# Optimization experiments

Hardware: AMD Instinct MI355X
Metric: run time of the kernel (lower is better)

Reference implementation:

```python
import jax, jax.numpy as jnp
import numpy as np

N = 50000
E = 800000
IN_C, HID, OUT_C = 128, 128, 40
EPS = 1e-5  # BatchNorm eps


def setup_inputs() -> dict:
    key = jax.random.key(0)
    ks = jax.random.split(key, 8)
    x = jax.random.normal(ks[0], (N, IN_C), dtype=jnp.float32)
    edge_index = jax.random.randint(ks[1], (2, E), 0, N, dtype=jnp.int64)
    s1 = 1.0 / np.sqrt(IN_C)
    s2 = 1.0 / np.sqrt(HID)
    return {
        "x": x,
        "edge_index": edge_index,
        "W1": jax.random.uniform(ks[2], (IN_C, HID), jnp.float32, -s1, s1),
        "b1": jnp.zeros((HID,), jnp.float32),
        "g1": jnp.ones((HID,), jnp.float32),
        "beta1": jnp.zeros((HID,), jnp.float32),
        "W2": jax.random.uniform(ks[3], (HID, HID), jnp.float32, -s2, s2),
        "b2": jnp.zeros((HID,), jnp.float32),
        "g2": jnp.ones((HID,), jnp.float32),
        "beta2": jnp.zeros((HID,), jnp.float32),
        "W3": jax.random.uniform(ks[4], (HID, OUT_C), jnp.float32, -s2, s2),
        "b3": jnp.zeros((OUT_C,), jnp.float32),
    }


def _gcn_norm(src, dst, num_nodes):
    # symmetric normalization D^-1/2 A D^-1/2, no self loops, unit edge weights
    deg = jax.ops.segment_sum(jnp.ones_like(dst, dtype=jnp.float32), dst,
                              num_segments=num_nodes)
    dinv = jnp.where(deg > 0, jax.lax.rsqrt(jnp.maximum(deg, 1.0)), 0.0)
    return dinv[src] * dinv[dst]  # [E]


def _conv(h, W, b, src, dst, norm, num_nodes):
    h = h @ W  # linear transform first (fewer message features)
    msg = norm[:, None] * h[src]  # [E, F] gather
    out = jax.ops.segment_sum(msg, dst, num_segments=num_nodes)  # scatter-add
    return out + b


def _bn_relu(h, g, beta):
    mu = jnp.mean(h, axis=0)
    var = jnp.mean(jnp.square(h - mu), axis=0)  # biased, as torch BN
    hn = (h - mu) * jax.lax.rsqrt(var + EPS) * g + beta
    return jax.nn.relu(hn)


def reference(x, edge_index, W1, b1, g1, beta1, W2, b2, g2, beta2, W3, b3):
    src, dst = edge_index[0], edge_index[1]
    norm = _gcn_norm(src, dst, N)  # cached=True: shared across layers
    h = _bn_relu(_conv(x, W1, b1, src, dst, norm, N), g1, beta1)
    h = _bn_relu(_conv(h, W2, b2, src, dst, norm, N), g2, beta2)
    return _conv(h, W3, b3, src, dst, norm, N)
```

## Files before the change

### kernel.cpp

```cpp
#include <hip/hip_runtime.h>
#include <hip/hip_fp16.h>

typedef _Float16 half8 __attribute__((ext_vector_type(8)));
typedef float floatx4 __attribute__((ext_vector_type(4)));


__device__ __forceinline__ void unpack8(uint4 v, float* f) {
    const __half2* hp = (const __half2*)&v;
    float2 a = __half22float2(hp[0]);
    float2 b = __half22float2(hp[1]);
    float2 c = __half22float2(hp[2]);
    float2 d = __half22float2(hp[3]);
    f[0] = a.x; f[1] = a.y; f[2] = b.x; f[3] = b.y;
    f[4] = c.x; f[5] = c.y; f[6] = d.x; f[7] = d.y;
}

__device__ __forceinline__ uint4 pack8(const float* f) {
    __half2 h0 = __floats2half2_rn(f[0], f[1]);
    __half2 h1 = __floats2half2_rn(f[2], f[3]);
    __half2 h2 = __floats2half2_rn(f[4], f[5]);
    __half2 h3 = __floats2half2_rn(f[6], f[7]);
    uint4 v;
    v.x = *(const unsigned int*)&h0;
    v.y = *(const unsigned int*)&h1;
    v.z = *(const unsigned int*)&h2;
    v.w = *(const unsigned int*)&h3;
    return v;
}

__global__ void k_zero4(float4* p, int n4) {
    int i = blockIdx.x * 256 + threadIdx.x;
    if (i < n4) p[i] = make_float4(0.f, 0.f, 0.f, 0.f);
}

__global__ void k_zeroi(int* p, int n) {
    int i = blockIdx.x * 256 + threadIdx.x;
    if (i < n) p[i] = 0;
}


__global__ void k_deg_xcd(const int* __restrict__ dst, int* __restrict__ deg,
                          int E, int rs) {
    int lo = (blockIdx.x & 7) * rs;
    int i = (blockIdx.x >> 3) * 256 + threadIdx.x;
    if (i < E) {
        int d = dst[i];
        if (d >= lo && d < lo + rs) atomicAdd(&deg[d], 1);
    }
}

__global__ void k_place_xcd(const int* __restrict__ src, const int* __restrict__ dst,
                            int* __restrict__ cursor, int* __restrict__ sidx,
                            int E, int rs) {
    int lo = (blockIdx.x & 7) * rs;
    int i = (blockIdx.x >> 3) * 256 + threadIdx.x;
    if (i < E) {
        int d = dst[i];
        if (d >= lo && d < lo + rs) {
            int pos = atomicAdd(&cursor[d], 1);
            sidx[pos] = src[i];
        }
    }
}

__global__ void k_dinv(const int* __restrict__ deg, float* __restrict__ dinv, int n) {
    int i = blockIdx.x * 256 + threadIdx.x;
    if (i < n) {
        int d = deg[i];
        dinv[i] = d > 0 ? rsqrtf((float)d) : 0.f;
    }
}

__global__ void k_blocksum(const int* __restrict__ cnt, int* __restrict__ bsum, int n) {
    __shared__ int ls[256];
    int i = blockIdx.x * 256 + threadIdx.x;
    ls[threadIdx.x] = i < n ? cnt[i] : 0;
    __syncthreads();
    for (int off = 128; off > 0; off >>= 1) {
        if (threadIdx.x < off) ls[threadIdx.x] += ls[threadIdx.x + off];
        __syncthreads();
    }
    if (threadIdx.x == 0) bsum[blockIdx.x] = ls[0];
}

__global__ void k_scanbsum(int* bsum, int nb) {
    if (threadIdx.x == 0 && blockIdx.x == 0) {
        int acc = 0;
        for (int i = 0; i < nb; ++i) { int v = bsum[i]; bsum[i] = acc; acc += v; }
    }
}

__global__ void k_scanchunk(const int* __restrict__ cnt, const int* __restrict__ bsum,
                            int* __restrict__ row_ptr, int* __restrict__ cursor,
                            int n, int E) {
    __shared__ int ls[256];
    int i = blockIdx.x * 256 + threadIdx.x;
    int v = i < n ? cnt[i] : 0;
    ls[threadIdx.x] = v;
    __syncthreads();
    for (int off = 1; off < 256; off <<= 1) {
        int t = threadIdx.x >= off ? ls[threadIdx.x - off] : 0;
        __syncthreads();
        ls[threadIdx.x] += t;
        __syncthreads();
    }
    if (i < n) {
        int ex = ls[threadIdx.x] - v + bsum[blockIdx.x];
        row_ptr[i] = ex;
        cursor[i] = ex;
    }
    if (i == n - 1) row_ptr[n] = E;
}


__global__ void k_packW(const float* __restrict__ W, __half* __restrict__ Wt,
                        int Nw, int Npad) {
    int i = blockIdx.x * 256 + threadIdx.x;
    if (i >= Npad * 128) return;
    int n = i >> 7, k = i & 127;
    Wt[i] = (n < Nw) ? __float2half(W[(size_t)k * Nw + n]) : __half(0.f);
}


template <int CT, int OUTW, int AMODE>
__global__ __launch_bounds__(256) void k_gemm_mfma(const void* __restrict__ Ap,
                                                   const __half* __restrict__ Wt,
                                                   const float* __restrict__ scale,
                                                   const float* __restrict__ shift,
                                                   const float* __restrict__ dinv,
                                                   __half* __restrict__ C, int nrows) {
    __shared__ char lw[CT * 16 * 256];
    __shared__ float lsc[128], lsh[128];
    const int nu4 = CT * 16 * 16;
    for (int i = threadIdx.x; i < nu4; i += 256) {
        int row = i >> 4, k8 = i & 15;
        uint4 v = ((const uint4*)Wt)[i];
        *(uint4*)(lw + ((row * 256 + k8 * 16) ^ ((row & 7) << 4))) = v;
    }
    if (AMODE == 1 && threadIdx.x < 128) {
        lsc[threadIdx.x] = scale[threadIdx.x];
        lsh[threadIdx.x] = shift[threadIdx.x];
    }
    __syncthreads();

    const int lane = threadIdx.x & 63;
    const int wid = threadIdx.x >> 6;
    const int l15 = lane & 15;
    const int lg = lane >> 4;
    const int rowbase = blockIdx.x * 128 + wid * 32;

    floatx4 acc[2][CT];
#pragma unroll
    for (int r = 0; r < 2; ++r)
#pragma unroll
        for (int c = 0; c < CT; ++c) acc[r][c] = (floatx4){0.f, 0.f, 0.f, 0.f};

    for (int kk = 0; kk < 4; ++kk) {
        half8 afrag[2];
        const int c0 = kk * 32 + lg * 8;
#pragma unroll
        for (int r = 0; r < 2; ++r) {
            int row = rowbase + r * 16 + l15;
            half8 h = {0, 0, 0, 0, 0, 0, 0, 0};
            if (row < nrows) {
                if (AMODE == 0) {
                    const float* a = (const float*)Ap + (size_t)row * 128 + c0;
                    float4 v0 = *(const float4*)a;
                    float4 v1 = *(const float4*)(a + 4);
                    h[0] = (_Float16)v0.x; h[1] = (_Float16)v0.y;
                    h[2] = (_Float16)v0.z; h[3] = (_Float16)v0.w;
                    h[4] = (_Float16)v1.x; h[5] = (_Float16)v1.y;
                    h[6] = (_Float16)v1.z; h[7] = (_Float16)v1.w;
                } else {
                    uint4 raw = *(const uint4*)((const __half*)Ap + (size_t)row * 128 + c0);
                    float f[8];
                    unpack8(raw, f);
                    float4 s0 = *(const float4*)&lsc[c0];
                    float4 s1 = *(const float4*)&lsc[c0 + 4];
                    float4 t0 = *(const float4*)&lsh[c0];
                    float4 t1 = *(const float4*)&lsh[c0 + 4];
                    h[0] = (_Float16)fmaxf(f[0] * s0.x + t0.x, 0.f);
                    h[1] = (_Float16)fmaxf(f[1] * s0.y + t0.y, 0.f);
                    h[2] = (_Float16)fmaxf(f[2] * s0.z + t0.z, 0.f);
                    h[3] = (_Float16)fmaxf(f[3] * s0.w + t0.w, 0.f);
                    h[4] = (_Float16)fmaxf(f[4] * s1.x + t1.x, 0.f);
                    h[5] = (_Float16)fmaxf(f[5] * s1.y + t1.y, 0.f);
                    h[6] = (_Float16)fmaxf(f[6] * s1.z + t1.z, 0.f);
                    h[7] = (_Float16)fmaxf(f[7] * s1.w + t1.w, 0.f);
                }
            }
            afrag[r] = h;
        }
#pragma unroll
        for (int c = 0; c < CT; ++c) {
            int wrow = c * 16 + l15;
            half8 bfrag = *(const half8*)(lw + ((wrow * 256 + kk * 64 + lg * 16) ^ ((wrow & 7) << 4)));
#pragma unroll
            for (int r = 0; r < 2; ++r)
                acc[r][c] = __builtin_amdgcn_mfma_f32_16x16x32_f16(afrag[r], bfrag, acc[r][c], 0, 0, 0);
        }
    }

#pragma unroll
    for (int r = 0; r < 2; ++r) {
        int rbase = rowbase + r * 16 + lg * 4;
        float d4[4];
#pragma unroll
        for (int j = 0; j < 4; ++j)
            d4[j] = (rbase + j) < nrows ? dinv[rbase + j] : 0.f;
#pragma unroll
        for (int c = 0; c < CT; ++c) {
            int col = c * 16 + l15;
            if (OUTW != CT * 16 && col >= OUTW) continue;
#pragma unroll
            for (int j = 0; j < 4; ++j) {
                int row = rbase + j;
                if (row < nrows)
                    C[(size_t)row * OUTW + col] = __float2half(acc[r][c][j] * d4[j]);
            }
        }
    }
}


__global__ __launch_bounds__(256) void k_agg128_stats(const __half* __restrict__ M,
                                                      const int* __restrict__ rp,
                                                      const int* __restrict__ sidx,
                                                      const float* __restrict__ dinv,
                                                      __half* __restrict__ Hout,
                                                      float* __restrict__ sums32,
                                                      float* __restrict__ sumsq32, int n) {
    int d = blockIdx.x * 16 + (threadIdx.x >> 4);
    int lane = threadIdx.x & 15;
    float acc[8] = {0.f, 0.f, 0.f, 0.f, 0.f, 0.f, 0.f, 0.f};
    if (d < n) {
        int beg = rp[d], end = rp[d + 1];
        int j = beg;
        for (; j + 4 <= end; j += 4) {
            int s0 = sidx[j], s1 = sidx[j + 1], s2 = sidx[j + 2], s3 = sidx[j + 3];
            uint4 v0 = *(const uint4*)(M + (size_t)s0 * 128 + lane * 8);
            uint4 v1 = *(const uint4*)(M + (size_t)s1 * 128 + lane * 8);
            uint4 v2 = *(const uint4*)(M + (size_t)s2 * 128 + lane * 8);
            uint4 v3 = *(const uint4*)(M + (size_t)s3 * 128 + lane * 8);
            float f0[8], f1[8], f2[8], f3[8];
            unpack8(v0, f0); unpack8(v1, f1); unpack8(v2, f2); unpack8(v3, f3);
#pragma unroll
            for (int i = 0; i < 8; ++i)
                acc[i] += (f0[i] + f1[i]) + (f2[i] + f3[i]);
        }
        for (; j < end; ++j) {
            int s = sidx[j];
            uint4 v = *(const uint4*)(M + (size_t)s * 128 + lane * 8);
            float f[8];
            unpack8(v, f);
#pragma unroll
            for (int i = 0; i < 8; ++i) acc[i] += f[i];
        }
        float sc = dinv[d];
#pragma unroll
        for (int i = 0; i < 8; ++i) acc[i] *= sc;
        *(uint4*)(Hout + (size_t)d * 128 + lane * 8) = pack8(acc);
    }
    float sq[8];
#pragma unroll
    for (int i = 0; i < 8; ++i) sq[i] = acc[i] * acc[i];
#pragma unroll
    for (int m = 16; m <= 32; m <<= 1) {
#pragma unroll
        for (int i = 0; i < 8; ++i) {
            acc[i] += __shfl_xor(acc[i], m);
            sq[i]  += __shfl_xor(sq[i], m);
        }
    }
    __shared__ float lsw[2][4][16][8];
    int wid = threadIdx.x >> 6, wl = threadIdx.x & 63;
    if (wl < 16) {
#pragma unroll
        for (int i = 0; i < 8; ++i) {
            lsw[0][wid][wl][i] = acc[i];
            lsw[1][wid][wl][i] = sq[i];
        }
    }
    __syncthreads();
    if (threadIdx.x < 128) {
        int c = threadIdx.x;
        int lc = c >> 3, e = c & 7;
        float ss = 0.f, qq = 0.f;
#pragma unroll
        for (int w = 0; w < 4; ++w) {
            ss += lsw[0][w][lc][e];
            qq += lsw[1][w][lc][e];
        }
        int sh = (blockIdx.x & 31) * 128;
        atomicAdd(&sums32[sh + c], ss);
        atomicAdd(&sumsq32[sh + c], qq);
    }
}

__global__ void k_bnfinal32(const float* __restrict__ sums32, const float* __restrict__ sumsq32,
                            const float* __restrict__ g, const float* __restrict__ beta,
                            float* __restrict__ scale, float* __restrict__ shift, int nrows) {
    int c = threadIdx.x;
    float s = 0.f, q = 0.f;
    for (int k = 0; k < 32; ++k) { s += sums32[k * 128 + c]; q += sumsq32[k * 128 + c]; }
    float inv_n = 1.f / (float)nrows;
    float mu = s * inv_n;
    float var = q * inv_n - mu * mu;
    float rs = rsqrtf(var + 1e-5f);
    float sc = rs * g[c];
    scale[c] = sc;
    shift[c] = beta[c] - mu * sc;
}


__global__ void k_agg40_f16(const __half* __restrict__ M,
                            const int* __restrict__ rp,
                            const int* __restrict__ sidx,
                            const float* __restrict__ dinv,
                            const float* __restrict__ b3,
                            float* __restrict__ out, int n) {
    int i = blockIdx.x * 256 + threadIdx.x;
    if (i >= n * 5) return;
    int d = i / 5, q = i % 5;
    int beg = rp[d], end = rp[d + 1];
    float acc[8] = {0.f, 0.f, 0.f, 0.f, 0.f, 0.f, 0.f, 0.f};
    int j = beg;
    for (; j + 4 <= end; j += 4) {
        int s0 = sidx[j], s1 = sidx[j + 1], s2 = sidx[j + 2], s3 = sidx[j + 3];
        uint4 v0 = *(const uint4*)(M + (size_t)s0 * 40 + q * 8);
        uint4 v1 = *(const uint4*)(M + (size_t)s1 * 40 + q * 8);
        uint4 v2 = *(const uint4*)(M + (size_t)s2 * 40 + q * 8);
        uint4 v3 = *(const uint4*)(M + (size_t)s3 * 40 + q * 8);
        float f0[8], f1[8], f2[8], f3[8];
        unpack8(v0, f0); unpack8(v1, f1); unpack8(v2, f2); unpack8(v3, f3);
#pragma unroll
        for (int k = 0; k < 8; ++k)
            acc[k] += (f0[k] + f1[k]) + (f2[k] + f3[k]);
    }
    for (; j < end; ++j) {
        int s = sidx[j];
        uint4 v = *(const uint4*)(M + (size_t)s * 40 + q * 8);
        float f[8];
        unpack8(v, f);
#pragma unroll
        for (int k = 0; k < 8; ++k) acc[k] += f[k];
    }
    float sc = dinv[d];
    float4 b0 = *(const float4*)&b3[q * 8];
    float4 b1 = *(const float4*)&b3[q * 8 + 4];
    float4 r0, r1;
    r0.x = acc[0] * sc + b0.x; r0.y = acc[1] * sc + b0.y;
    r0.z = acc[2] * sc + b0.z; r0.w = acc[3] * sc + b0.w;
    r1.x = acc[4] * sc + b1.x; r1.y = acc[5] * sc + b1.y;
    r1.z = acc[6] * sc + b1.z; r1.w = acc[7] * sc + b1.w;
    float* o = out + (size_t)d * 40 + q * 8;
    *(float4*)o = r0;
    *(float4*)(o + 4) = r1;
}


extern "C" void kernel_launch(void* const* d_in, const int* in_sizes, int n_in,
                              void* d_out, int out_size, void* d_ws, size_t ws_size,
                              hipStream_t stream) {
    const float* x  = (const float*)d_in[0];
    const int*   ei = (const int*)d_in[1];
    const float* W1 = (const float*)d_in[2];
    const float* g1 = (const float*)d_in[4];
    const float* be1= (const float*)d_in[5];
    const float* W2 = (const float*)d_in[6];
    const float* g2 = (const float*)d_in[8];
    const float* be2= (const float*)d_in[9];
    const float* W3 = (const float*)d_in[10];
    const float* b3 = (const float*)d_in[11];

    const int N = in_sizes[0] / 128;
    const int E = in_sizes[1] / 2;
    const int* srcv = ei;
    const int* dstv = ei + E;
    const int NB = (N + 255) / 256;
    const int RS = (N + 7) / 8;
    const int EB8 = 8 * ((E + 255) / 256);

    __half* M    = (__half*)d_ws;
    __half* Hb   = M + (size_t)N * 128;
    __half* t3   = Hb + (size_t)N * 128;
    __half* Wt1  = t3 + (size_t)N * 40;
    __half* Wt2  = Wt1 + 128 * 128;
    __half* Wt3  = Wt2 + 128 * 128;
    float* dinv    = (float*)(Wt3 + 48 * 128);
    int*   deg     = (int*)(dinv + N);
    int*   row_ptr = deg + N;
    int*   cursor  = row_ptr + N + 1;
    int*   sidx    = cursor + N;
    int*   bsum    = sidx + E;
    float* sums32  = (float*)(bsum + NB + 1);
    float* sumsq32 = sums32 + 32 * 128;
    float* scale   = sumsq32 + 32 * 128;
    float* shift   = scale + 128;
    float* out     = (float*)d_out;

    const int GB = (N + 127) / 128;

    k_packW<<<(128 * 128 + 255) / 256, 256, 0, stream>>>(W1, Wt1, 128, 128);
    k_packW<<<(128 * 128 + 255) / 256, 256, 0, stream>>>(W2, Wt2, 128, 128);
    k_packW<<<(48 * 128 + 255) / 256, 256, 0, stream>>>(W3, Wt3, 40, 48);

    k_zeroi<<<(N + 255) / 256, 256, 0, stream>>>(deg, N);
    k_deg_xcd<<<EB8, 256, 0, stream>>>(dstv, deg, E, RS);
    k_dinv<<<(N + 255) / 256, 256, 0, stream>>>(deg, dinv, N);
    k_blocksum<<<NB, 256, 0, stream>>>(deg, bsum, N);
    k_scanbsum<<<1, 64, 0, stream>>>(bsum, NB);
    k_scanchunk<<<NB, 256, 0, stream>>>(deg, bsum, row_ptr, cursor, N, E);
    k_place_xcd<<<EB8, 256, 0, stream>>>(srcv, dstv, cursor, sidx, E, RS);

    k_zero4<<<(2048 + 255) / 256, 256, 0, stream>>>((float4*)sums32, 2048);
    k_gemm_mfma<8, 128, 0><<<GB, 256, 0, stream>>>(x, Wt1, nullptr, nullptr, dinv, M, N);
    k_agg128_stats<<<(N + 15) / 16, 256, 0, stream>>>(M, row_ptr, sidx, dinv, Hb, sums32, sumsq32, N);
    k_bnfinal32<<<1, 128, 0, stream>>>(sums32, sumsq32, g1, be1, scale, shift, N);

    k_gemm_mfma<8, 128, 1><<<GB, 256, 0, stream>>>(Hb, Wt2, scale, shift, dinv, M, N);
    k_zero4<<<(2048 + 255) / 256, 256, 0, stream>>>((float4*)sums32, 2048);
    k_agg128_stats<<<(N + 15) / 16, 256, 0, stream>>>(M, row_ptr, sidx, dinv, Hb, sums32, sumsq32, N);
    k_bnfinal32<<<1, 128, 0, stream>>>(sums32, sumsq32, g2, be2, scale, shift, N);

    k_gemm_mfma<3, 40, 1><<<GB, 256, 0, stream>>>(Hb, Wt3, scale, shift, dinv, t3, N);
    k_agg40_f16<<<(N * 5 + 255) / 256, 256, 0, stream>>>(t3, row_ptr, sidx, dinv, b3, out, N);
}
```

Measured before the change: 247.4 us.

## Cut kernel launches by merging setup kernels and folding BN finalization into GEMM

Merges the three weight-pack kernels into one, folds the dinv computation into the scan kernel, replaces the blocksum and serial scan pair with a single one-block chunk scan, and zeroes degrees and both BN stat buffers in one launch. The BN finalize kernels are removed: each GEMM block now reduces the 32 partial sums itself, using separate buffers per layer. The layer-3 intermediate is padded to a 64-half row stride so gathered rows are 128-byte aligned. This trades fewer launches and less serial work for a redundant per-block stats reduction and a larger t3 buffer.

```diff
diff --git a/kernel.cpp b/kernel.cpp
--- a/kernel.cpp
+++ b/kernel.cpp
@@ -28,14 +28,28 @@
     return v;
 }
 
-__global__ void k_zero4(float4* p, int n4) {
-    int i = blockIdx.x * 256 + threadIdx.x;
-    if (i < n4) p[i] = make_float4(0.f, 0.f, 0.f, 0.f);
-}
-
-__global__ void k_zeroi(int* p, int n) {
+__global__ void k_zeroz(int* p, int n) {
     int i = blockIdx.x * 256 + threadIdx.x;
     if (i < n) p[i] = 0;
+}
+
+
+__global__ void k_packW3(const float* __restrict__ W1, const float* __restrict__ W2,
+                         const float* __restrict__ W3, __half* __restrict__ Wt1,
+                         __half* __restrict__ Wt2, __half* __restrict__ Wt3) {
+    int i = blockIdx.x * 256 + threadIdx.x;
+    if (i < 128 * 128) {
+        int n = i >> 7, k = i & 127;
+        Wt1[i] = __float2half(W1[(size_t)k * 128 + n]);
+    } else if (i < 2 * 128 * 128) {
+        int j = i - 128 * 128;
+        int n = j >> 7, k = j & 127;
+        Wt2[j] = __float2half(W2[(size_t)k * 128 + n]);
+    } else if (i < 2 * 128 * 128 + 48 * 128) {
+        int j = i - 2 * 128 * 128;
+        int n = j >> 7, k = j & 127;
+        Wt3[j] = (n < 40) ? __float2half(W3[(size_t)k * 40 + n]) : __half(0.f);
+    }
 }
 
 
@@ -63,36 +77,30 @@
     }
 }
 
-__global__ void k_dinv(const int* __restrict__ deg, float* __restrict__ dinv, int n) {
-    int i = blockIdx.x * 256 + threadIdx.x;
-    if (i < n) {
-        int d = deg[i];
-        dinv[i] = d > 0 ? rsqrtf((float)d) : 0.f;
-    }
-}
-
-__global__ void k_blocksum(const int* __restrict__ cnt, int* __restrict__ bsum, int n) {
+__global__ __launch_bounds__(256) void k_chunkscan(const int* __restrict__ deg,
+                                                   int* __restrict__ bsum, int n) {
     __shared__ int ls[256];
-    int i = blockIdx.x * 256 + threadIdx.x;
-    ls[threadIdx.x] = i < n ? cnt[i] : 0;
+    int t = threadIdx.x;
+    int s = 0;
+    int base = t * 256;
+    for (int k = 0; k < 256; ++k) {
+        int idx = base + k;
+        if (idx < n) s += deg[idx];
+    }
+    ls[t] = s;
     __syncthreads();
-    for (int off = 128; off > 0; off >>= 1) {
-        if (threadIdx.x < off) ls[threadIdx.x] += ls[threadIdx.x + off];
+    for (int off = 1; off < 256; off <<= 1) {
+        int v = t >= off ? ls[t - off] : 0;
         __syncthreads();
-    }
-    if (threadIdx.x == 0) bsum[blockIdx.x] = ls[0];
-}
-
-__global__ void k_scanbsum(int* bsum, int nb) {
-    if (threadIdx.x == 0 && blockIdx.x == 0) {
-        int acc = 0;
-        for (int i = 0; i < nb; ++i) { int v = bsum[i]; bsum[i] = acc; acc += v; }
-    }
+        ls[t] += v;
+        __syncthreads();
+    }
+    bsum[t] = ls[t] - s;
 }
 
 __global__ void k_scanchunk(const int* __restrict__ cnt, const int* __restrict__ bsum,
                             int* __restrict__ row_ptr, int* __restrict__ cursor,
-                            int n, int E) {
+                            float* __restrict__ dinv, int n, int E) {
     __shared__ int ls[256];
     int i = blockIdx.x * 256 + threadIdx.x;
     int v = i < n ? cnt[i] : 0;
@@ -108,25 +116,19 @@
         int ex = ls[threadIdx.x] - v + bsum[blockIdx.x];
         row_ptr[i] = ex;
         cursor[i] = ex;
+        dinv[i] = v > 0 ? rsqrtf((float)v) : 0.f;
     }
     if (i == n - 1) row_ptr[n] = E;
 }
 
 
-__global__ void k_packW(const float* __restrict__ W, __half* __restrict__ Wt,
-                        int Nw, int Npad) {
-    int i = blockIdx.x * 256 + threadIdx.x;
-    if (i >= Npad * 128) return;
-    int n = i >> 7, k = i & 127;
-    Wt[i] = (n < Nw) ? __float2half(W[(size_t)k * Nw + n]) : __half(0.f);
-}
-
-
-template <int CT, int OUTW, int AMODE>
+template <int CT, int STRIDE, int VALID, int AMODE>
 __global__ __launch_bounds__(256) void k_gemm_mfma(const void* __restrict__ Ap,
                                                    const __half* __restrict__ Wt,
-                                                   const float* __restrict__ scale,
-                                                   const float* __restrict__ shift,
+                                                   const float* __restrict__ sums32,
+                                                   const float* __restrict__ sumsq32,
+                                                   const float* __restrict__ g,
+                                                   const float* __restrict__ beta,
                                                    const float* __restrict__ dinv,
                                                    __half* __restrict__ C, int nrows) {
     __shared__ char lw[CT * 16 * 256];
@@ -138,8 +140,19 @@
         *(uint4*)(lw + ((row * 256 + k8 * 16) ^ ((row & 7) << 4))) = v;
     }
     if (AMODE == 1 && threadIdx.x < 128) {
-        lsc[threadIdx.x] = scale[threadIdx.x];
-        lsh[threadIdx.x] = shift[threadIdx.x];
+        int c = threadIdx.x;
+        float s = 0.f, q = 0.f;
+        for (int k2 = 0; k2 < 32; ++k2) {
+            s += sums32[k2 * 128 + c];
+            q += sumsq32[k2 * 128 + c];
+        }
+        float inv_n = 1.f / (float)nrows;
+        float mu = s * inv_n;
+        float var = q * inv_n - mu * mu;
+        float rs = rsqrtf(var + 1e-5f);
+        float sc = rs * g[c];
+        lsc[c] = sc;
+        lsh[c] = beta[c] - mu * sc;
     }
     __syncthreads();
 
@@ -211,12 +224,12 @@
 #pragma unroll
         for (int c = 0; c < CT; ++c) {
             int col = c * 16 + l15;
-            if (OUTW != CT * 16 && col >= OUTW) continue;
+            if (VALID != CT * 16 && col >= VALID) continue;
 #pragma unroll
             for (int j = 0; j < 4; ++j) {
                 int row = rbase + j;
                 if (row < nrows)
-                    C[(size_t)row * OUTW + col] = __float2half(acc[r][c][j] * d4[j]);
+                    C[(size_t)row * STRIDE + col] = __float2half(acc[r][c][j] * d4[j]);
             }
         }
     }
@@ -297,21 +310,6 @@
     }
 }
 
-__global__ void k_bnfinal32(const float* __restrict__ sums32, const float* __restrict__ sumsq32,
-                            const float* __restrict__ g, const float* __restrict__ beta,
-                            float* __restrict__ scale, float* __restrict__ shift, int nrows) {
-    int c = threadIdx.x;
-    float s = 0.f, q = 0.f;
-    for (int k = 0; k < 32; ++k) { s += sums32[k * 128 + c]; q += sumsq32[k * 128 + c]; }
-    float inv_n = 1.f / (float)nrows;
-    float mu = s * inv_n;
-    float var = q * inv_n - mu * mu;
-    float rs = rsqrtf(var + 1e-5f);
-    float sc = rs * g[c];
-    scale[c] = sc;
-    shift[c] = beta[c] - mu * sc;
-}
-
 
 __global__ void k_agg40_f16(const __half* __restrict__ M,
                             const int* __restrict__ rp,
@@ -327,10 +325,10 @@
     int j = beg;
     for (; j + 4 <= end; j += 4) {
         int s0 = sidx[j], s1 = sidx[j + 1], s2 = sidx[j + 2], s3 = sidx[j + 3];
-        uint4 v0 = *(const uint4*)(M + (size_t)s0 * 40 + q * 8);
-        uint4 v1 = *(const uint4*)(M + (size_t)s1 * 40 + q * 8);
-        uint4 v2 = *(const uint4*)(M + (size_t)s2 * 40 + q * 8);
-        uint4 v3 = *(const uint4*)(M + (size_t)s3 * 40 + q * 8);
+        uint4 v0 = *(const uint4*)(M + (size_t)s0 * 64 + q * 8);
+        uint4 v1 = *(const uint4*)(M + (size_t)s1 * 64 + q * 8);
+        uint4 v2 = *(const uint4*)(M + (size_t)s2 * 64 + q * 8);
+        uint4 v3 = *(const uint4*)(M + (size_t)s3 * 64 + q * 8);
         float f0[8], f1[8], f2[8], f3[8];
         unpack8(v0, f0); unpack8(v1, f1); unpack8(v2, f2); unpack8(v3, f3);
 #pragma unroll
@@ -339,7 +337,7 @@
     }
     for (; j < end; ++j) {
         int s = sidx[j];
-        uint4 v = *(const uint4*)(M + (size_t)s * 40 + q * 8);
+        uint4 v = *(const uint4*)(M + (size_t)s * 64 + q * 8);
         float f[8];
         unpack8(v, f);
 #pragma unroll
@@ -384,45 +382,37 @@
     __half* M    = (__half*)d_ws;
     __half* Hb   = M + (size_t)N * 128;
     __half* t3   = Hb + (size_t)N * 128;
-    __half* Wt1  = t3 + (size_t)N * 40;
+    __half* Wt1  = t3 + (size_t)N * 64;
     __half* Wt2  = Wt1 + 128 * 128;
     __half* Wt3  = Wt2 + 128 * 128;
     float* dinv    = (float*)(Wt3 + 48 * 128);
     int*   deg     = (int*)(dinv + N);
-    int*   row_ptr = deg + N;
+    float* sumsA   = (float*)(deg + N);
+    float* sumsqA  = sumsA + 32 * 128;
+    float* sumsB   = sumsqA + 32 * 128;
+    float* sumsqB  = sumsB + 32 * 128;
+    int*   row_ptr = (int*)(sumsqB + 32 * 128);
     int*   cursor  = row_ptr + N + 1;
     int*   sidx    = cursor + N;
     int*   bsum    = sidx + E;
-    float* sums32  = (float*)(bsum + NB + 1);
-    float* sumsq32 = sums32 + 32 * 128;
-    float* scale   = sumsq32 + 32 * 128;
-    float* shift   = scale + 128;
     float* out     = (float*)d_out;
 
     const int GB = (N + 127) / 128;
-
-    k_packW<<<(128 * 128 + 255) / 256, 256, 0, stream>>>(W1, Wt1, 128, 128);
-    k_packW<<<(128 * 128 + 255) / 256, 256, 0, stream>>>(W2, Wt2, 128, 128);
-    k_packW<<<(48 * 128 + 255) / 256, 256, 0, stream>>>(W3, Wt3, 40, 48);
-
-    k_zeroi<<<(N + 255) / 256, 256, 0, stream>>>(deg, N);
+    const int ZN = N + 4 * 32 * 128;
+
+    k_packW3<<<(2 * 128 * 128 + 48 * 128 + 255) / 256, 256, 0, stream>>>(W1, W2, W3, Wt1, Wt2, Wt3);
+    k_zeroz<<<(ZN + 255) / 256, 256, 0, stream>>>(deg, ZN);
     k_deg_xcd<<<EB8, 256, 0, stream>>>(dstv, deg, E, RS);
-    k_dinv<<<(N + 255) / 256, 256, 0, stream>>>(deg, dinv, N);
-    k_blocksum<<<NB, 256, 0, stream>>>(deg, bsum, N);
-    k_scanbsum<<<1, 64, 0, stream>>>(bsum, NB);
-    k_scanchunk<<<NB, 256, 0, stream>>>(deg, bsum, row_ptr, cursor, N, E);
+    k_chunkscan<<<1, 256, 0, stream>>>(deg, bsum, N);
+    k_scanchunk<<<NB, 256, 0, stream>>>(deg, bsum, row_ptr, cursor, dinv, N, E);
     k_place_xcd<<<EB8, 256, 0, stream>>>(srcv, dstv, cursor, sidx, E, RS);
 
-    k_zero4<<<(2048 + 255) / 256, 256, 0, stream>>>((float4*)sums32, 2048);
-    k_gemm_mfma<8, 128, 0><<<GB, 256, 0, stream>>>(x, Wt1, nullptr, nullptr, dinv, M, N);
-    k_agg128_stats<<<(N + 15) / 16, 256, 0, stream>>>(M, row_ptr, sidx, dinv, Hb, sums32, sumsq32, N);
-    k_bnfinal32<<<1, 128, 0, stream>>>(sums32, sumsq32, g1, be1, scale, shift, N);
-
-    k_gemm_mfma<8, 128, 1><<<GB, 256, 0, stream>>>(Hb, Wt2, scale, shift, dinv, M, N);
-    k_zero4<<<(2048 + 255) / 256, 256, 0, stream>>>((float4*)sums32, 2048);
-    k_agg128_stats<<<(N + 15) / 16, 256, 0, stream>>>(M, row_ptr, sidx, dinv, Hb, sums32, sumsq32, N);
-    k_bnfinal32<<<1, 128, 0, stream>>>(sums32, sumsq32, g2, be2, scale, shift, N);
-
-    k_gemm_mfma<3, 40, 1><<<GB, 256, 0, stream>>>(Hb, Wt3, scale, shift, dinv, t3, N);
+    k_gemm_mfma<8, 128, 128, 0><<<GB, 256, 0, stream>>>(x, Wt1, nullptr, nullptr, nullptr, nullptr, dinv, M, N);
+    k_agg128_stats<<<(N + 15) / 16, 256, 0, stream>>>(M, row_ptr, sidx, dinv, Hb, sumsA, sumsqA, N);
+
+    k_gemm_mfma<8, 128, 128, 1><<<GB, 256, 0, stream>>>(Hb, Wt2, sumsA, sumsqA, g1, be1, dinv, M, N);
+    k_agg128_stats<<<(N + 15) / 16, 256, 0, stream>>>(M, row_ptr, sidx, dinv, Hb, sumsB, sumsqB, N);
+
+    k_gemm_mfma<3, 64, 40, 1><<<GB, 256, 0, stream>>>(Hb, Wt3, sumsB, sumsqB, g2, be2, dinv, t3, N);
     k_agg40_f16<<<(N * 5 + 255) / 256, 256, 0, stream>>>(t3, row_ptr, sidx, dinv, b3, out, N);
 }
```

Result: faster. 241.0 us (-2.6%).
